# Kernel optimization log

Hardware: AMD Instinct MI355X
Metric: run time of the kernel (lower is better)

## Reference

```python
import jax, jax.numpy as jnp
import numpy as np

DIM = 1024
BLOCK = 64
N_BLOCKS = DIM // BLOCK
N = 65536
INIT_SCALE = 0.01


def setup_inputs() -> dict:
    key = jax.random.key(0)
    k1, k2 = jax.random.split(key)
    x = jax.random.normal(k1, (N, DIM), dtype=jnp.float32)
    skew_params = jax.random.normal(k2, (N_BLOCKS, BLOCK, BLOCK), dtype=jnp.float32) * INIT_SCALE
    perm = jnp.asarray(np.random.default_rng(0).permutation(DIM), dtype=jnp.int64)
    return {"x": x, "skew_params": skew_params, "perm": perm}


def reference(x, skew_params, perm):
    # Skew-symmetrize each block: A = P - P^T, shape [K, b, b]
    A = skew_params - jnp.swapaxes(skew_params, -1, -2)
    # Per-block orthogonal matrices via matrix exponential, [K, b, b]
    B = jax.vmap(jax.scipy.linalg.expm)(A)
    # Block-diagonal matmul without materializing the dense [dim, dim] matrix:
    # x @ block_diag(B_0..B_{K-1}) == batched per-block matmul on reshaped x.
    xb = x.reshape(x.shape[0], N_BLOCKS, BLOCK)          # [N, K, b]
    yb = jnp.einsum("nkb,kbc->nkc", xb, B)               # [N, K, b]
    y = yb.reshape(x.shape[0], DIM)                      # [N, dim]
    # Shuffle: column permutation
    return y[:, perm]
```

## Files before the change

### kernel.cpp

```cpp
#include <hip/hip_runtime.h>

#define DIM           1024
#define BLK           64
#define NB            16
#define RT            16
#define MAIN_THREADS  512
#define NWG           512
#define NTILES        4096
#define P68           68
#define BFRAG_STRIDE  512

typedef float  f32x4  __attribute__((ext_vector_type(4)));
typedef short  bf16x8 __attribute__((ext_vector_type(8)));

static __device__ __forceinline__ short f2bf(float f) {
    union { float f; unsigned u; } v; v.f = f;
    unsigned r = v.u + 0x7fffu + ((v.u >> 16) & 1u);
    return (short)(r >> 16);
}

static __device__ __forceinline__ void gload16(const float* g, void* l) {
    __builtin_amdgcn_global_load_lds(
        (const __attribute__((address_space(1))) unsigned int*)g,
        (__attribute__((address_space(3))) unsigned int*)l, 16, 0, 0);
}

__global__ void decode_perm_kernel(const int* __restrict__ praw,
                                   int* __restrict__ pout) {
    __shared__ int zc;
    if (threadIdx.x == 0) zc = 0;
    __syncthreads();
    int local = 0;
    for (int i = threadIdx.x; i < DIM; i += blockDim.x)
        if (praw[i] == 0) local++;
    if (local) atomicAdd(&zc, local);
    __syncthreads();
    const bool is64 = (zc > 100);
    const long long* p64 = (const long long*)praw;
    for (int i = threadIdx.x; i < DIM; i += blockDim.x)
        pout[i] = is64 ? (int)p64[i] : praw[i];
}

__global__ __launch_bounds__(512) void expm_kernel(
        const float* __restrict__ skew, ushort* __restrict__ Btl) {
    __shared__ float Asm[BLK][P68];
    __shared__ float Tb[2][BLK][P68];
    __shared__ float Rm[BLK][P68];
    const int k   = blockIdx.x;
    const int tid = threadIdx.x;
    const float* P = skew + (size_t)k * (BLK * BLK);

    for (int e = tid; e < BLK * BLK; e += 512) {
        const int i = e >> 6, j = e & 63;
        const float a = P[i * BLK + j] - P[j * BLK + i];
        Asm[i][j]   = a;
        Tb[0][i][j] = a;
        Rm[i][j]    = a + (i == j ? 1.0f : 0.0f);
    }
    __syncthreads();

    const int i0 = (tid >> 4) * 2;
    const int j0 = (tid & 15) * 4;

    for (int n = 2; n <= 7; ++n) {
        const float invn = 1.0f / (float)n;
        const float (*Tc)[P68] = Tb[n & 1];
        float       (*Tn)[P68] = Tb[1 - (n & 1)];
        f32x4 acc0 = {0.f, 0.f, 0.f, 0.f}, acc1 = {0.f, 0.f, 0.f, 0.f};
        for (int b = 0; b < BLK; ++b) {
            const f32x4 av = *(const f32x4*)&Asm[b][j0];
            acc0 += Tc[i0][b]     * av;
            acc1 += Tc[i0 + 1][b] * av;
        }
        acc0 *= invn; acc1 *= invn;
        *(f32x4*)&Tn[i0][j0]     = acc0;
        *(f32x4*)&Tn[i0 + 1][j0] = acc1;
        f32x4 r0 = *(const f32x4*)&Rm[i0][j0];     r0 += acc0; *(f32x4*)&Rm[i0][j0]     = r0;
        f32x4 r1 = *(const f32x4*)&Rm[i0 + 1][j0]; r1 += acc1; *(f32x4*)&Rm[i0 + 1][j0] = r1;
        __syncthreads();
    }

    for (int e = tid; e < BLK * BLK; e += 512) {
        const int b = e >> 6, c = e & 63;
        const int n = c >> 4, m = c & 15;
        const int h = b >> 5, g = (b >> 3) & 3, j = b & 7;
        const size_t idx = (size_t)((k * 4 + n) * 2 + h) * BFRAG_STRIDE
                         + g * 128 + m * 8 + j;
        Btl[idx] = (ushort)f2bf(Rm[b][c]);
    }
}

__global__ __launch_bounds__(MAIN_THREADS, 4) void gsl_main_kernel(
        const float* __restrict__ x, const ushort* __restrict__ Btl,
        const int* __restrict__ perm, float* __restrict__ out) {
    __shared__ float xy[16384];
    __shared__ int   plds[DIM];

    const int tid  = threadIdx.x;
    const int lane = tid & 63;
    const int w    = tid >> 6;
    const int g    = lane >> 4;
    const int m16  = lane & 15;

    for (int i = tid; i < DIM; i += MAIN_THREADS) plds[i] = perm[i];

    bf16x8 bf[2][4][2];
#pragma unroll
    for (int b = 0; b < 2; ++b) {
        const int k = w + 8 * b;
#pragma unroll
        for (int n = 0; n < 4; ++n)
#pragma unroll
            for (int h = 0; h < 2; ++h)
                bf[b][n][h] = *(const bf16x8*)(Btl +
                    (size_t)((k * 4 + n) * 2 + h) * BFRAG_STRIDE + lane * 8);
    }

    char* const xyb = (char*)xy;

    const int srow  = tid >> 5;
    const int sslot = (tid & 31) ^ (srow & 7);
    char* const ldst0 = xyb + tid * 16;

    for (int it = 0; it < NTILES / NWG; ++it) {
        const int    tile = blockIdx.x + it * NWG;
        const size_t r0   = (size_t)tile * RT;

        if (it) __syncthreads();
        const float* gsrc = x + (r0 + srow) * DIM + sslot * 4;
#pragma unroll
        for (int s = 0; s < 8; ++s)
            gload16(gsrc + s * 128, ldst0 + s * 8192);
        __syncthreads();

#pragma unroll
        for (int b = 0; b < 2; ++b) {
            const int k  = w + 8 * b;
            const int k2 = k >> 1;
            const int sb = (k & 1) * 16;
            const char* rowp = xyb + k2 * 8192 + m16 * 512;
            const int   xs   = m16 & 7;
            const f32x4 a0 = *(const f32x4*)(rowp + (((sb + 2 * g    ) ^ xs) << 4));
            const f32x4 a1 = *(const f32x4*)(rowp + (((sb + 2 * g + 1) ^ xs) << 4));
            const f32x4 a2 = *(const f32x4*)(rowp + (((sb + 8 + 2 * g    ) ^ xs) << 4));
            const f32x4 a3 = *(const f32x4*)(rowp + (((sb + 8 + 2 * g + 1) ^ xs) << 4));
            bf16x8 alo, ahi;
            alo[0] = f2bf(a0[0]); alo[1] = f2bf(a0[1]); alo[2] = f2bf(a0[2]); alo[3] = f2bf(a0[3]);
            alo[4] = f2bf(a1[0]); alo[5] = f2bf(a1[1]); alo[6] = f2bf(a1[2]); alo[7] = f2bf(a1[3]);
            ahi[0] = f2bf(a2[0]); ahi[1] = f2bf(a2[1]); ahi[2] = f2bf(a2[2]); ahi[3] = f2bf(a2[3]);
            ahi[4] = f2bf(a3[0]); ahi[5] = f2bf(a3[1]); ahi[6] = f2bf(a3[2]); ahi[7] = f2bf(a3[3]);

            f32x4 acc[4];
#pragma unroll
            for (int n = 0; n < 4; ++n) acc[n] = (f32x4){0.f, 0.f, 0.f, 0.f};
#pragma unroll
            for (int n = 0; n < 4; ++n)
                acc[n] = __builtin_amdgcn_mfma_f32_16x16x32_bf16(alo, bf[b][n][0], acc[n], 0, 0, 0);
#pragma unroll
            for (int n = 0; n < 4; ++n)
                acc[n] = __builtin_amdgcn_mfma_f32_16x16x32_bf16(ahi, bf[b][n][1], acc[n], 0, 0, 0);

#pragma unroll
            for (int n = 0; n < 4; ++n) {
                const int c    = sb * 4 + n * 16 + m16;
                const int slot = c >> 2;
                const int d    = (c & 3) * 4;
#pragma unroll
                for (int i = 0; i < 4; ++i) {
                    const int row = g * 4 + i;
                    *(float*)(xyb + k2 * 8192 + row * 512 +
                              (((slot ^ (row & 7)) << 4)) + d) = acc[n][i];
                }
            }
        }
        __syncthreads();

        const int   r   = tid >> 5;
        const int   q   = tid & 31;
        const int   rx  = r & 7;
        const char* rb  = xyb + r * 512;
        float*      orow = out + (r0 + r) * DIM;
#pragma unroll
        for (int i2 = 0; i2 < 8; ++i2) {
            const int c4 = (q + 32 * i2) << 2;
            f32x4 v;
#pragma unroll
            for (int u = 0; u < 4; ++u) {
                const int p = plds[c4 + u];
                v[u] = *(const float*)(rb + (p >> 7) * 8192 +
                                       ((((p >> 2) & 31) ^ rx) << 4) + (p & 3) * 4);
            }
            *(f32x4*)(orow + c4) = v;
        }
    }
}

extern "C" void kernel_launch(void* const* d_in, const int* in_sizes, int n_in,
                              void* d_out, int out_size, void* d_ws, size_t ws_size,
                              hipStream_t stream) {
    const float* x    = (const float*)d_in[0];
    const float* skew = (const float*)d_in[1];
    const int*   perm = (const int*)d_in[2];
    float* out = (float*)d_out;

    ushort* Btl    = (ushort*)d_ws;
    int*    perm_i = (int*)((char*)d_ws + (size_t)NB * BLK * BLK * sizeof(ushort));

    decode_perm_kernel<<<1, 256, 0, stream>>>(perm, perm_i);
    expm_kernel<<<NB, 512, 0, stream>>>(skew, Btl);
    gsl_main_kernel<<<NWG, MAIN_THREADS, 0, stream>>>(x, Btl, perm_i, out);
}
```

Baseline: 142.0 us.

## Double-buffer x tiles in LDS and fold perm decode into expm launch

The main kernel now runs 256 persistent workgroups, each handling 16 contiguous tiles. Two LDS buffers let the async global-to-LDS load of the next tile overlap compute and the permuted epilogue of the current tile, with manual vmcnt/lgkmcnt waits and raw barriers. Occupancy drops to 2 workgroups per CU because LDS use doubles. The separate perm decode launch is merged into an extra block of the expm kernel to save one launch.

```diff
diff --git a/kernel.cpp b/kernel.cpp
--- a/kernel.cpp
+++ b/kernel.cpp
@@ -5,8 +5,8 @@
 #define NB            16
 #define RT            16
 #define MAIN_THREADS  512
-#define NWG           512
-#define NTILES        4096
+#define NWG           256
+#define NT            16
 #define P68           68
 #define BFRAG_STRIDE  512
 
@@ -25,29 +25,37 @@
         (__attribute__((address_space(3))) unsigned int*)l, 16, 0, 0);
 }
 
-__global__ void decode_perm_kernel(const int* __restrict__ praw,
-                                   int* __restrict__ pout) {
-    __shared__ int zc;
-    if (threadIdx.x == 0) zc = 0;
-    __syncthreads();
-    int local = 0;
-    for (int i = threadIdx.x; i < DIM; i += blockDim.x)
-        if (praw[i] == 0) local++;
-    if (local) atomicAdd(&zc, local);
-    __syncthreads();
-    const bool is64 = (zc > 100);
-    const long long* p64 = (const long long*)praw;
-    for (int i = threadIdx.x; i < DIM; i += blockDim.x)
-        pout[i] = is64 ? (int)p64[i] : praw[i];
-}
+#define WAITV8()  asm volatile("s_waitcnt vmcnt(8)"  ::: "memory")
+#define WAITV16() asm volatile("s_waitcnt vmcnt(16)" ::: "memory")
+#define WAITL()   asm volatile("s_waitcnt lgkmcnt(0)" ::: "memory")
+#define SBAR()    __builtin_amdgcn_s_barrier()
+#define SCHED0()  __builtin_amdgcn_sched_barrier(0)
 
 __global__ __launch_bounds__(512) void expm_kernel(
-        const float* __restrict__ skew, ushort* __restrict__ Btl) {
+        const float* __restrict__ skew, ushort* __restrict__ Btl,
+        const int* __restrict__ praw, int* __restrict__ pout) {
     __shared__ float Asm[BLK][P68];
     __shared__ float Tb[2][BLK][P68];
     __shared__ float Rm[BLK][P68];
-    const int k   = blockIdx.x;
     const int tid = threadIdx.x;
+
+    if (blockIdx.x == NB) {
+        __shared__ int zc;
+        if (tid == 0) zc = 0;
+        __syncthreads();
+        int local = 0;
+        for (int i = tid; i < DIM; i += 512)
+            if (praw[i] == 0) local++;
+        if (local) atomicAdd(&zc, local);
+        __syncthreads();
+        const bool is64 = (zc > 100);
+        const long long* p64 = (const long long*)praw;
+        for (int i = tid; i < DIM; i += 512)
+            pout[i] = is64 ? (int)p64[i] : praw[i];
+        return;
+    }
+
+    const int k = blockIdx.x;
     const float* P = skew + (size_t)k * (BLK * BLK);
 
     for (int e = tid; e < BLK * BLK; e += 512) {
@@ -90,10 +98,11 @@
     }
 }
 
-__global__ __launch_bounds__(MAIN_THREADS, 4) void gsl_main_kernel(
+__global__ __launch_bounds__(MAIN_THREADS, 2) void gsl_main_kernel(
         const float* __restrict__ x, const ushort* __restrict__ Btl,
         const int* __restrict__ perm, float* __restrict__ out) {
-    __shared__ float xy[16384];
+    __shared__ float xy0[16384];
+    __shared__ float xy1[16384];
     __shared__ int   plds[DIM];
 
     const int tid  = threadIdx.x;
@@ -116,23 +125,21 @@
                     (size_t)((k * 4 + n) * 2 + h) * BFRAG_STRIDE + lane * 8);
     }
 
-    char* const xyb = (char*)xy;
-
     const int srow  = tid >> 5;
     const int sslot = (tid & 31) ^ (srow & 7);
-    char* const ldst0 = xyb + tid * 16;
-
-    for (int it = 0; it < NTILES / NWG; ++it) {
-        const int    tile = blockIdx.x + it * NWG;
-        const size_t r0   = (size_t)tile * RT;
-
-        if (it) __syncthreads();
+    const int tile0 = blockIdx.x * NT;
+
+    auto stage = [&](int it, float* buf) {
+        const size_t r0   = (size_t)(tile0 + it) * RT;
         const float* gsrc = x + (r0 + srow) * DIM + sslot * 4;
+        char*        ldst = (char*)buf + tid * 16;
 #pragma unroll
         for (int s = 0; s < 8; ++s)
-            gload16(gsrc + s * 128, ldst0 + s * 8192);
-        __syncthreads();
-
+            gload16(gsrc + s * 128, ldst + s * 8192);
+    };
+
+    auto compute = [&](float* buf) {
+        char* const xyb = (char*)buf;
 #pragma unroll
         for (int b = 0; b < 2; ++b) {
             const int k  = w + 8 * b;
@@ -173,13 +180,14 @@
                 }
             }
         }
-        __syncthreads();
-
-        const int   r   = tid >> 5;
-        const int   q   = tid & 31;
-        const int   rx  = r & 7;
-        const char* rb  = xyb + r * 512;
-        float*      orow = out + (r0 + r) * DIM;
+    };
+
+    auto epilogue = [&](int it, const float* buf) {
+        const size_t r0  = (size_t)(tile0 + it) * RT;
+        const int    q   = tid & 31;
+        const int    rx  = srow & 7;
+        const char*  rb  = (const char*)buf + srow * 512;
+        float*       orow = out + (r0 + srow) * DIM;
 #pragma unroll
         for (int i2 = 0; i2 < 8; ++i2) {
             const int c4 = (q + 32 * i2) << 2;
@@ -192,7 +200,31 @@
             }
             *(f32x4*)(orow + c4) = v;
         }
-    }
+    };
+
+    stage(0, xy0);
+
+    stage(1, xy1);
+    WAITV8(); SBAR();
+    compute(xy0);
+    WAITL(); SBAR();
+
+    for (int it = 1; it < NT - 1; ++it) {
+        float* Xc = (it & 1) ? xy1 : xy0;
+        float* Xn = (it & 1) ? xy0 : xy1;
+        epilogue(it - 1, Xn);
+        WAITL(); SCHED0();
+        stage(it + 1, Xn);
+        WAITV16(); SBAR();
+        compute(Xc);
+        WAITL(); SBAR();
+    }
+
+    epilogue(NT - 2, xy0);
+    WAITV8(); SBAR();
+    compute(xy1);
+    WAITL(); SBAR();
+    epilogue(NT - 1, xy1);
 }
 
 extern "C" void kernel_launch(void* const* d_in, const int* in_sizes, int n_in,
@@ -206,7 +238,6 @@
     ushort* Btl    = (ushort*)d_ws;
     int*    perm_i = (int*)((char*)d_ws + (size_t)NB * BLK * BLK * sizeof(ushort));
 
-    decode_perm_kernel<<<1, 256, 0, stream>>>(perm, perm_i);
-    expm_kernel<<<NB, 512, 0, stream>>>(skew, Btl);
+    expm_kernel<<<NB + 1, 512, 0, stream>>>(skew, Btl, perm, perm_i);
     gsl_main_kernel<<<NWG, MAIN_THREADS, 0, stream>>>(x, Btl, perm_i, out);
 }
```

New measurement: 134.9 us. 1.05x faster.

## Restructure main kernel: direct register x loads, inverse-perm scatter, double-buffered LDS

Applied to the files above, without the earlier changes.

The main kernel now uses 1024-thread workgroups, one wave per 64-wide block, and each workgroup handles 16 consecutive tiles. x is loaded straight into registers and prefetched one tile ahead, replacing the global-to-LDS staging. MFMA results are scattered into a double-buffered LDS tile at positions given by the inverse permutation, so the output can be written as contiguous rows, and the store of each tile overlaps the compute of the next with a single barrier per iteration. The permutation decode is merged into the expm launch as an extra block that builds the inverse permutation, which removes one kernel launch. The cost is more LDS per workgroup, lower occupancy, and uncoalesced direct global loads of x.

```diff
diff --git a/kernel.cpp b/kernel.cpp
--- a/kernel.cpp
+++ b/kernel.cpp
@@ -4,9 +4,9 @@
 #define BLK           64
 #define NB            16
 #define RT            16
-#define MAIN_THREADS  512
-#define NWG           512
-#define NTILES        4096
+#define MAIN_THREADS  1024
+#define NWG           256
+#define NT            16
 #define P68           68
 #define BFRAG_STRIDE  512
 
@@ -19,35 +19,36 @@
     return (short)(r >> 16);
 }
 
-static __device__ __forceinline__ void gload16(const float* g, void* l) {
-    __builtin_amdgcn_global_load_lds(
-        (const __attribute__((address_space(1))) unsigned int*)g,
-        (__attribute__((address_space(3))) unsigned int*)l, 16, 0, 0);
-}
-
-__global__ void decode_perm_kernel(const int* __restrict__ praw,
-                                   int* __restrict__ pout) {
-    __shared__ int zc;
-    if (threadIdx.x == 0) zc = 0;
-    __syncthreads();
-    int local = 0;
-    for (int i = threadIdx.x; i < DIM; i += blockDim.x)
-        if (praw[i] == 0) local++;
-    if (local) atomicAdd(&zc, local);
-    __syncthreads();
-    const bool is64 = (zc > 100);
-    const long long* p64 = (const long long*)praw;
-    for (int i = threadIdx.x; i < DIM; i += blockDim.x)
-        pout[i] = is64 ? (int)p64[i] : praw[i];
-}
+#define WAITL()   asm volatile("s_waitcnt lgkmcnt(0)" ::: "memory")
+#define SBAR()    __builtin_amdgcn_s_barrier()
 
 __global__ __launch_bounds__(512) void expm_kernel(
-        const float* __restrict__ skew, ushort* __restrict__ Btl) {
+        const float* __restrict__ skew, ushort* __restrict__ Btl,
+        const int* __restrict__ praw, int* __restrict__ pinv) {
     __shared__ float Asm[BLK][P68];
     __shared__ float Tb[2][BLK][P68];
     __shared__ float Rm[BLK][P68];
-    const int k   = blockIdx.x;
     const int tid = threadIdx.x;
+
+    if (blockIdx.x == NB) {
+        __shared__ int zc;
+        if (tid == 0) zc = 0;
+        __syncthreads();
+        int local = 0;
+        for (int i = tid; i < DIM; i += 512)
+            if (praw[i] == 0) local++;
+        if (local) atomicAdd(&zc, local);
+        __syncthreads();
+        const bool is64 = (zc > 100);
+        const long long* p64 = (const long long*)praw;
+        for (int i = tid; i < DIM; i += 512) {
+            const int v = is64 ? (int)p64[i] : praw[i];
+            pinv[v] = i;
+        }
+        return;
+    }
+
+    const int k = blockIdx.x;
     const float* P = skew + (size_t)k * (BLK * BLK);
 
     for (int e = tid; e < BLK * BLK; e += 512) {
@@ -90,11 +91,10 @@
     }
 }
 
-__global__ __launch_bounds__(MAIN_THREADS, 4) void gsl_main_kernel(
+__global__ __launch_bounds__(MAIN_THREADS) void gsl_main_kernel(
         const float* __restrict__ x, const ushort* __restrict__ Btl,
-        const int* __restrict__ perm, float* __restrict__ out) {
-    __shared__ float xy[16384];
-    __shared__ int   plds[DIM];
+        const int* __restrict__ pinv, float* __restrict__ out) {
+    __shared__ float yb[2][16384];
 
     const int tid  = threadIdx.x;
     const int lane = tid & 63;
@@ -102,95 +102,91 @@
     const int g    = lane >> 4;
     const int m16  = lane & 15;
 
-    for (int i = tid; i < DIM; i += MAIN_THREADS) plds[i] = perm[i];
-
-    bf16x8 bf[2][4][2];
-#pragma unroll
-    for (int b = 0; b < 2; ++b) {
-        const int k = w + 8 * b;
+    bf16x8 bfr[4][2];
+#pragma unroll
+    for (int n = 0; n < 4; ++n)
+#pragma unroll
+        for (int h = 0; h < 2; ++h)
+            bfr[n][h] = *(const bf16x8*)(Btl +
+                (size_t)((w * 4 + n) * 2 + h) * BFRAG_STRIDE + lane * 8);
+
+    int sbase[4], sx3[4];
+#pragma unroll
+    for (int n = 0; n < 4; ++n) {
+        const int c  = w * 64 + n * 16 + m16;
+        const int j  = pinv[c];
+        const int g4 = j >> 2;
+        sbase[n] = g4 * 256 + (((4 * g) ^ (g4 & 12)) << 4) + (j & 3) * 4;
+        sx3[n]   = g4 & 3;
+    }
+
+    const int tile0 = blockIdx.x * NT;
+    const float* xw = x + w * 64 + g * 8;
+
+    f32x4 a0, a1, a2, a3;
+    {
+        const float* xp = xw + (size_t)(tile0 * RT + m16) * DIM;
+        a0 = *(const f32x4*)(xp);      a1 = *(const f32x4*)(xp + 4);
+        a2 = *(const f32x4*)(xp + 32); a3 = *(const f32x4*)(xp + 36);
+    }
+
+    for (int it = 0; it < NT; ++it) {
+        float*       yc = yb[it & 1];
+        const float* yp = yb[(it & 1) ^ 1];
+
+        bf16x8 alo, ahi;
+        alo[0] = f2bf(a0[0]); alo[1] = f2bf(a0[1]); alo[2] = f2bf(a0[2]); alo[3] = f2bf(a0[3]);
+        alo[4] = f2bf(a1[0]); alo[5] = f2bf(a1[1]); alo[6] = f2bf(a1[2]); alo[7] = f2bf(a1[3]);
+        ahi[0] = f2bf(a2[0]); ahi[1] = f2bf(a2[1]); ahi[2] = f2bf(a2[2]); ahi[3] = f2bf(a2[3]);
+        ahi[4] = f2bf(a3[0]); ahi[5] = f2bf(a3[1]); ahi[6] = f2bf(a3[2]); ahi[7] = f2bf(a3[3]);
+
+        if (it + 1 < NT) {
+            const float* xp = xw + (size_t)((tile0 + it + 1) * RT + m16) * DIM;
+            a0 = *(const f32x4*)(xp);      a1 = *(const f32x4*)(xp + 4);
+            a2 = *(const f32x4*)(xp + 32); a3 = *(const f32x4*)(xp + 36);
+        }
+
+        f32x4 acc[4];
+#pragma unroll
+        for (int n = 0; n < 4; ++n) acc[n] = (f32x4){0.f, 0.f, 0.f, 0.f};
 #pragma unroll
         for (int n = 0; n < 4; ++n)
-#pragma unroll
-            for (int h = 0; h < 2; ++h)
-                bf[b][n][h] = *(const bf16x8*)(Btl +
-                    (size_t)((k * 4 + n) * 2 + h) * BFRAG_STRIDE + lane * 8);
-    }
-
-    char* const xyb = (char*)xy;
-
-    const int srow  = tid >> 5;
-    const int sslot = (tid & 31) ^ (srow & 7);
-    char* const ldst0 = xyb + tid * 16;
-
-    for (int it = 0; it < NTILES / NWG; ++it) {
-        const int    tile = blockIdx.x + it * NWG;
-        const size_t r0   = (size_t)tile * RT;
-
-        if (it) __syncthreads();
-        const float* gsrc = x + (r0 + srow) * DIM + sslot * 4;
-#pragma unroll
-        for (int s = 0; s < 8; ++s)
-            gload16(gsrc + s * 128, ldst0 + s * 8192);
-        __syncthreads();
-
-#pragma unroll
-        for (int b = 0; b < 2; ++b) {
-            const int k  = w + 8 * b;
-            const int k2 = k >> 1;
-            const int sb = (k & 1) * 16;
-            const char* rowp = xyb + k2 * 8192 + m16 * 512;
-            const int   xs   = m16 & 7;
-            const f32x4 a0 = *(const f32x4*)(rowp + (((sb + 2 * g    ) ^ xs) << 4));
-            const f32x4 a1 = *(const f32x4*)(rowp + (((sb + 2 * g + 1) ^ xs) << 4));
-            const f32x4 a2 = *(const f32x4*)(rowp + (((sb + 8 + 2 * g    ) ^ xs) << 4));
-            const f32x4 a3 = *(const f32x4*)(rowp + (((sb + 8 + 2 * g + 1) ^ xs) << 4));
-            bf16x8 alo, ahi;
-            alo[0] = f2bf(a0[0]); alo[1] = f2bf(a0[1]); alo[2] = f2bf(a0[2]); alo[3] = f2bf(a0[3]);
-            alo[4] = f2bf(a1[0]); alo[5] = f2bf(a1[1]); alo[6] = f2bf(a1[2]); alo[7] = f2bf(a1[3]);
-            ahi[0] = f2bf(a2[0]); ahi[1] = f2bf(a2[1]); ahi[2] = f2bf(a2[2]); ahi[3] = f2bf(a2[3]);
-            ahi[4] = f2bf(a3[0]); ahi[5] = f2bf(a3[1]); ahi[6] = f2bf(a3[2]); ahi[7] = f2bf(a3[3]);
-
-            f32x4 acc[4];
-#pragma unroll
-            for (int n = 0; n < 4; ++n) acc[n] = (f32x4){0.f, 0.f, 0.f, 0.f};
-#pragma unroll
-            for (int n = 0; n < 4; ++n)
-                acc[n] = __builtin_amdgcn_mfma_f32_16x16x32_bf16(alo, bf[b][n][0], acc[n], 0, 0, 0);
-#pragma unroll
-            for (int n = 0; n < 4; ++n)
-                acc[n] = __builtin_amdgcn_mfma_f32_16x16x32_bf16(ahi, bf[b][n][1], acc[n], 0, 0, 0);
-
-#pragma unroll
-            for (int n = 0; n < 4; ++n) {
-                const int c    = sb * 4 + n * 16 + m16;
-                const int slot = c >> 2;
-                const int d    = (c & 3) * 4;
-#pragma unroll
-                for (int i = 0; i < 4; ++i) {
-                    const int row = g * 4 + i;
-                    *(float*)(xyb + k2 * 8192 + row * 512 +
-                              (((slot ^ (row & 7)) << 4)) + d) = acc[n][i];
-                }
+            acc[n] = __builtin_amdgcn_mfma_f32_16x16x32_bf16(alo, bfr[n][0], acc[n], 0, 0, 0);
+#pragma unroll
+        for (int n = 0; n < 4; ++n)
+            acc[n] = __builtin_amdgcn_mfma_f32_16x16x32_bf16(ahi, bfr[n][1], acc[n], 0, 0, 0);
+
+        char* const ycb = (char*)yc;
+#pragma unroll
+        for (int n = 0; n < 4; ++n)
+#pragma unroll
+            for (int i = 0; i < 4; ++i)
+                *(float*)(ycb + sbase[n] + ((i ^ sx3[n]) << 4)) = acc[n][i];
+
+        if (it) {
+            const char* ypb  = (const char*)yp;
+            float*      orow = out + (size_t)((tile0 + it - 1) * RT + w) * DIM;
+#pragma unroll
+            for (int i2 = 0; i2 < 4; ++i2) {
+                const int j4   = lane + 64 * i2;
+                const int slot = w ^ (j4 & 15);
+                const f32x4 v  = *(const f32x4*)(ypb + j4 * 256 + slot * 16);
+                *(f32x4*)(orow + j4 * 4) = v;
             }
         }
-        __syncthreads();
-
-        const int   r   = tid >> 5;
-        const int   q   = tid & 31;
-        const int   rx  = r & 7;
-        const char* rb  = xyb + r * 512;
-        float*      orow = out + (r0 + r) * DIM;
-#pragma unroll
-        for (int i2 = 0; i2 < 8; ++i2) {
-            const int c4 = (q + 32 * i2) << 2;
-            f32x4 v;
-#pragma unroll
-            for (int u = 0; u < 4; ++u) {
-                const int p = plds[c4 + u];
-                v[u] = *(const float*)(rb + (p >> 7) * 8192 +
-                                       ((((p >> 2) & 31) ^ rx) << 4) + (p & 3) * 4);
-            }
-            *(f32x4*)(orow + c4) = v;
+
+        WAITL(); SBAR();
+    }
+
+    {
+        const char* ypb  = (const char*)yb[(NT - 1) & 1];
+        float*      orow = out + (size_t)((tile0 + NT - 1) * RT + w) * DIM;
+#pragma unroll
+        for (int i2 = 0; i2 < 4; ++i2) {
+            const int j4   = lane + 64 * i2;
+            const int slot = w ^ (j4 & 15);
+            const f32x4 v  = *(const f32x4*)(ypb + j4 * 256 + slot * 16);
+            *(f32x4*)(orow + j4 * 4) = v;
         }
     }
 }
@@ -203,10 +199,9 @@
     const int*   perm = (const int*)d_in[2];
     float* out = (float*)d_out;
 
-    ushort* Btl    = (ushort*)d_ws;
-    int*    perm_i = (int*)((char*)d_ws + (size_t)NB * BLK * BLK * sizeof(ushort));
-
-    decode_perm_kernel<<<1, 256, 0, stream>>>(perm, perm_i);
-    expm_kernel<<<NB, 512, 0, stream>>>(skew, Btl);
-    gsl_main_kernel<<<NWG, MAIN_THREADS, 0, stream>>>(x, Btl, perm_i, out);
-}
+    ushort* Btl  = (ushort*)d_ws;
+    int*    pinv = (int*)((char*)d_ws + (size_t)NB * BLK * BLK * sizeof(ushort));
+
+    expm_kernel<<<NB + 1, 512, 0, stream>>>(skew, Btl, perm, pinv);
+    gsl_main_kernel<<<NWG, MAIN_THREADS, 0, stream>>>(x, Btl, pinv, out);
+}
```

After: 131.0 us. 7.7% less time.
